# Kernel tuning notes

Measured on AMD Instinct MI355X. Metric: run time of the kernel, lower is better.

The kernel has to match this reference:

```python
import jax, jax.numpy as jnp
import numpy as np

S, D = 8192, 2048      # sequence length, feature dim (input_size)
H, E, K, L = 64, 64, 2, 64  # gate hidden, expert count, top-k, expert layer_size
EPS = 1e-12            # torch F.normalize eps


def setup_inputs() -> dict:
    key = jax.random.key(0)
    ks = jax.random.split(key, 5)
    x = jax.random.normal(ks[0], (S, D), dtype=jnp.float32)
    # torch nn.Linear weights have shape [out_features, in_features]
    Wg_in = jax.random.normal(ks[1], (H, D), dtype=jnp.float32) * 0.02   # gate.input
    Wg_lin = jax.random.normal(ks[2], (E, H), dtype=jnp.float32) * 0.02  # gate.linear
    Wg_out = jax.random.normal(ks[3], (1, S), dtype=jnp.float32) * 0.02  # gate.output
    We = jax.random.normal(ks[4], (E, L, D), dtype=jnp.float32) * 0.02   # expert weight bank
    return {"x": x, "Wg_in": Wg_in, "Wg_lin": Wg_lin, "Wg_out": Wg_out, "We": We}


def reference(x, Wg_in, Wg_lin, Wg_out, We):
    # --- SparseGate (eval mode: dropout = identity) ---
    h = x @ Wg_in.T                         # [S, H]
    logits = h @ Wg_lin.T                   # [S, E]
    scores = (logits.T @ Wg_out.T)[:, 0]    # Linear(S,1) applied to [E,S] -> [E]
    topv, idx = jax.lax.top_k(scores, K)    # global top-k experts for whole input
    g = jax.nn.softmax(topv)                # softmax over the k selected logits

    # --- dispatch to k selected experts (FFNN: Linear -> normalize(-1) -> GELU) ---
    Wsel = We[idx]                          # [K, L, D]
    z = jnp.einsum('sd,kld->ksl', x, Wsel)  # [K, S, L]
    z = z / jnp.maximum(jnp.linalg.norm(z, axis=-1, keepdims=True), EPS)
    z = jax.nn.gelu(z, approximate=False)   # torch GELU default is exact erf

    # --- weighted combine: sum_k g_k * expert_k(x) ---
    return jnp.einsum('k,ksl->sl', g, z)    # [S, L]
```

## Files before the change

### kernel.cpp

```cpp
#include <hip/hip_runtime.h>
#include <hip/hip_bf16.h>
#include <math.h>

#define D_DIM 2048
#define L_DIM 64
#define E_NUM 64
#define H_DIM 64

typedef float f32x4_t __attribute__((ext_vector_type(4)));
typedef __bf16 bf16x8_t __attribute__((ext_vector_type(8)));

#define WS_UPART 0u
#define WS_U     (128u * 2048u * 4u)
#define WS_V     (WS_U + 2048u * 4u)
#define WS_META  (WS_V + 256u)
#define WS_WB    (WS_META + 64u)

__global__ void k_upart(const float* __restrict__ x, const float* __restrict__ wout,
                        float* __restrict__ upart) {
  const int d4 = (blockIdx.x * 256 + threadIdx.x) * 4;
  const int s0 = blockIdx.y * 64;
  const float* xp = x + (size_t)s0 * D_DIM + d4;
  float4 acc = make_float4(0.f, 0.f, 0.f, 0.f);
#pragma unroll 8
  for (int i = 0; i < 64; ++i) {
    const float w = wout[s0 + i];
    const float4 xv = *reinterpret_cast<const float4*>(xp + (size_t)i * D_DIM);
    acc.x += xv.x * w; acc.y += xv.y * w; acc.z += xv.z * w; acc.w += xv.w * w;
  }
  *reinterpret_cast<float4*>(upart + (size_t)blockIdx.y * D_DIM + d4) = acc;
}

__global__ void k_ufinish(const float* __restrict__ upart, float* __restrict__ u) {
  const int d = blockIdx.x * 256 + threadIdx.x;
  float s = 0.f;
#pragma unroll 8
  for (int c = 0; c < 128; ++c) s += upart[(size_t)c * D_DIM + d];
  u[d] = s;
}

__global__ void k_v(const float* __restrict__ wg_in, const float* __restrict__ u,
                    float* __restrict__ v) {
  const int h = blockIdx.x;
  const int t = threadIdx.x;
  const float4* wr = reinterpret_cast<const float4*>(wg_in + (size_t)h * D_DIM);
  const float4* ur = reinterpret_cast<const float4*>(u);
  float s = 0.f;
#pragma unroll
  for (int i = t; i < 512; i += 256) {
    const float4 a = wr[i];
    const float4 b = ur[i];
    s += a.x * b.x + a.y * b.y + a.z * b.z + a.w * b.w;
  }
  __shared__ float red[4];
#pragma unroll
  for (int off = 32; off; off >>= 1) s += __shfl_down(s, off, 64);
  if ((t & 63) == 0) red[t >> 6] = s;
  __syncthreads();
  if (t == 0) v[h] = red[0] + red[1] + red[2] + red[3];
}

__global__ void k_gate(const float* __restrict__ wg_lin, const float* __restrict__ v,
                       int* __restrict__ sel, float* __restrict__ g) {
  __shared__ float vv[H_DIM];
  __shared__ float sc[E_NUM];
  const int t = threadIdx.x;
  vv[t] = v[t];
  __syncthreads();
  float s = 0.f;
#pragma unroll 8
  for (int hh = 0; hh < H_DIM; ++hh) s += wg_lin[t * H_DIM + hh] * vv[hh];
  sc[t] = s;
  __syncthreads();
  if (t == 0) {
    int b1 = 0; float m1 = sc[0];
    for (int e = 1; e < E_NUM; ++e) { if (sc[e] > m1) { m1 = sc[e]; b1 = e; } }
    int b2 = -1; float m2 = -3.4e38f;
    for (int e = 0; e < E_NUM; ++e) {
      if (e != b1 && sc[e] > m2) { m2 = sc[e]; b2 = e; }
    }
    const float e2 = expf(m2 - m1);
    const float g0 = 1.0f / (1.0f + e2);
    sel[0] = b1; sel[1] = b2;
    g[0] = g0; g[1] = 1.0f - g0;
  }
}

__global__ void k_wb(const float* __restrict__ we, const int* __restrict__ sel,
                     __hip_bfloat16* __restrict__ wb) {
  const int n = blockIdx.x;
  const int e = sel[n >> 6];
  const int l = n & 63;
  const float* src = we + ((size_t)e * L_DIM + l) * D_DIM;
  const int t = threadIdx.x;
  const float4 a = reinterpret_cast<const float4*>(src)[2 * t];
  const float4 b = reinterpret_cast<const float4*>(src)[2 * t + 1];
  union { __hip_bfloat16 h[8]; uint4 u; } pk;
  pk.h[0] = __float2bfloat16(a.x); pk.h[1] = __float2bfloat16(a.y);
  pk.h[2] = __float2bfloat16(a.z); pk.h[3] = __float2bfloat16(a.w);
  pk.h[4] = __float2bfloat16(b.x); pk.h[5] = __float2bfloat16(b.y);
  pk.h[6] = __float2bfloat16(b.z); pk.h[7] = __float2bfloat16(b.w);
  reinterpret_cast<uint4*>(wb + (size_t)n * D_DIM)[t] = pk.u;
}

__device__ __forceinline__ void async_ld16(const void* gp, void* lp) {
  __builtin_amdgcn_global_load_lds(
      (const __attribute__((address_space(1))) unsigned int*)gp,
      (__attribute__((address_space(3))) unsigned int*)lp, 16, 0, 0);
}

__device__ __forceinline__ float gelu_f(float v) {
  return 0.5f * v * (1.0f + erff(v * 0.70710678118654752440f));
}

__global__ __launch_bounds__(256) void k_moe_gemm(
    const float* __restrict__ x, const __hip_bfloat16* __restrict__ wb,
    const float* __restrict__ gw, float* __restrict__ out) {
  __shared__ __align__(16) unsigned char lds[32 * 144 + 128 * 64 * 2];
  unsigned char* ldsA0 = lds;
  unsigned char* ldsB0 = lds + 32 * 144;

  const int tid = threadIdx.x;
  const int wv = tid >> 6;
  const int lane = tid & 63;
  const int m0 = blockIdx.x * 32;
  const float g0 = gw[0], g1 = gw[1];

  const int ar = tid >> 3, ac = tid & 7;
  const float* gA = x + (size_t)(m0 + ar) * D_DIM + ac * 8;
  unsigned char* ldsAw = ldsA0 + ar * 144 + ac * 16;

  const int fr = lane & 15, fq = lane >> 4;

  f32x4_t acc00 = {0.f, 0.f, 0.f, 0.f};
  f32x4_t acc01 = acc00, acc10 = acc00, acc11 = acc00;

  for (int kk = 0; kk < D_DIM / 64; ++kk) {
    const int k0 = kk * 64;
    if (kk) __syncthreads();
    const float4 a0 = *reinterpret_cast<const float4*>(gA + k0);
    const float4 a1 = *reinterpret_cast<const float4*>(gA + k0 + 4);
    union { __hip_bfloat16 h[8]; uint4 u; } pk;
    pk.h[0] = __float2bfloat16(a0.x); pk.h[1] = __float2bfloat16(a0.y);
    pk.h[2] = __float2bfloat16(a0.z); pk.h[3] = __float2bfloat16(a0.w);
    pk.h[4] = __float2bfloat16(a1.x); pk.h[5] = __float2bfloat16(a1.y);
    pk.h[6] = __float2bfloat16(a1.z); pk.h[7] = __float2bfloat16(a1.w);
    *reinterpret_cast<uint4*>(ldsAw) = pk.u;
#pragma unroll
    for (int i = 0; i < 4; ++i) {
      const int c = i * 256 + tid;
      const int r = c >> 3, p = c & 7;
      const int kc = p ^ (r & 7);
      async_ld16(wb + (size_t)r * D_DIM + k0 + kc * 8, ldsB0 + c * 16);
    }
    __syncthreads();
    union fragu { uint4 u; bf16x8_t v; };
    fragu af[2][2], bfr[2][2];
#pragma unroll
    for (int mt = 0; mt < 2; ++mt)
#pragma unroll
      for (int ks = 0; ks < 2; ++ks)
        af[mt][ks].u = *reinterpret_cast<const uint4*>(
            ldsA0 + (mt * 16 + fr) * 144 + ks * 64 + fq * 16);
#pragma unroll
    for (int nt = 0; nt < 2; ++nt)
#pragma unroll
      for (int ks = 0; ks < 2; ++ks) {
        const int r = wv * 32 + nt * 16 + fr;
        const int kg = ks * 4 + fq;
        bfr[nt][ks].u = *reinterpret_cast<const uint4*>(
            ldsB0 + r * 128 + ((kg ^ (r & 7)) * 16));
      }
    acc00 = __builtin_amdgcn_mfma_f32_16x16x32_bf16(af[0][0].v, bfr[0][0].v, acc00, 0, 0, 0);
    acc00 = __builtin_amdgcn_mfma_f32_16x16x32_bf16(af[0][1].v, bfr[0][1].v, acc00, 0, 0, 0);
    acc01 = __builtin_amdgcn_mfma_f32_16x16x32_bf16(af[0][0].v, bfr[1][0].v, acc01, 0, 0, 0);
    acc01 = __builtin_amdgcn_mfma_f32_16x16x32_bf16(af[0][1].v, bfr[1][1].v, acc01, 0, 0, 0);
    acc10 = __builtin_amdgcn_mfma_f32_16x16x32_bf16(af[1][0].v, bfr[0][0].v, acc10, 0, 0, 0);
    acc10 = __builtin_amdgcn_mfma_f32_16x16x32_bf16(af[1][1].v, bfr[0][1].v, acc10, 0, 0, 0);
    acc11 = __builtin_amdgcn_mfma_f32_16x16x32_bf16(af[1][0].v, bfr[1][0].v, acc11, 0, 0, 0);
    acc11 = __builtin_amdgcn_mfma_f32_16x16x32_bf16(af[1][1].v, bfr[1][1].v, acc11, 0, 0, 0);
  }
  __syncthreads();
  float* z = reinterpret_cast<float*>(lds);
  {
    const int colbase = wv * 32 + fr;
#pragma unroll
    for (int reg = 0; reg < 4; ++reg) {
      const int r0 = fq * 4 + reg;
      z[r0 * 132 + colbase]             = acc00[reg];
      z[r0 * 132 + colbase + 16]        = acc01[reg];
      z[(16 + r0) * 132 + colbase]      = acc10[reg];
      z[(16 + r0) * 132 + colbase + 16] = acc11[reg];
    }
  }
  __syncthreads();
  float* ps = reinterpret_cast<float*>(lds + 16896);
  {
    const int r = tid >> 3, seg = tid & 7;
    float s = 0.f;
#pragma unroll
    for (int i2 = 0; i2 < 16; ++i2) {
      const float t2 = z[r * 132 + seg * 16 + i2];
      s += t2 * t2;
    }
    ps[r * 8 + seg] = s;
  }
  __syncthreads();
  {
    const int r = tid >> 3, j = tid & 7;
    const float s0 = ps[r * 8 + 0] + ps[r * 8 + 1] + ps[r * 8 + 2] + ps[r * 8 + 3];
    const float s1 = ps[r * 8 + 4] + ps[r * 8 + 5] + ps[r * 8 + 6] + ps[r * 8 + 7];
    const float i0 = 1.0f / fmaxf(sqrtf(s0), 1e-12f);
    const float i1 = 1.0f / fmaxf(sqrtf(s1), 1e-12f);
    float o[8];
#pragma unroll
    for (int i2 = 0; i2 < 8; ++i2) {
      const int c = j * 8 + i2;
      const float za = z[r * 132 + c] * i0;
      const float zb = z[r * 132 + 64 + c] * i1;
      o[i2] = g0 * gelu_f(za) + g1 * gelu_f(zb);
    }
    float4* op = reinterpret_cast<float4*>(out + (size_t)(m0 + r) * 64 + j * 8);
    op[0] = make_float4(o[0], o[1], o[2], o[3]);
    op[1] = make_float4(o[4], o[5], o[6], o[7]);
  }
}

extern "C" void kernel_launch(void* const* d_in, const int* in_sizes, int n_in,
                              void* d_out, int out_size, void* d_ws, size_t ws_size,
                              hipStream_t stream) {
  (void)in_sizes; (void)n_in; (void)out_size; (void)ws_size;
  const float* x      = (const float*)d_in[0];
  const float* wg_in  = (const float*)d_in[1];
  const float* wg_lin = (const float*)d_in[2];
  const float* wg_out = (const float*)d_in[3];
  const float* we     = (const float*)d_in[4];
  float* out = (float*)d_out;
  char* ws = (char*)d_ws;

  float* upart = (float*)(ws + WS_UPART);
  float* u     = (float*)(ws + WS_U);
  float* v     = (float*)(ws + WS_V);
  int*   sel   = (int*)(ws + WS_META);
  float* g     = (float*)(ws + WS_META + 8);
  __hip_bfloat16* wb = (__hip_bfloat16*)(ws + WS_WB);

  k_upart  <<<dim3(2, 128), 256, 0, stream>>>(x, wg_out, upart);
  k_ufinish<<<8, 256, 0, stream>>>(upart, u);
  k_v      <<<64, 256, 0, stream>>>(wg_in, u, v);
  k_gate   <<<1, 64, 0, stream>>>(wg_lin, v, sel, g);
  k_wb     <<<128, 256, 0, stream>>>(we, sel, wb);
  k_moe_gemm<<<256, 256, 0, stream>>>(x, wb, g, out);
}
```

Before: 169.0 us.

## Split GEMM K dimension across four wave groups per block with LDS reduction

The MoE GEMM block grows from 256 to 1024 threads. Each group of 256 threads handles a quarter of the 2048-long reduction using its own LDS staging region, and the partial results are summed in LDS before normalization and GELU. The goal is more in-flight memory traffic and MFMA work per CU with only 256 blocks, which shortens the serial K loop per block. In exchange it adds an LDS reduction step, a larger shared-memory footprint that can lower occupancy, and an epilogue where only a quarter of the threads do work.

```diff
diff --git a/kernel.cpp b/kernel.cpp
--- a/kernel.cpp
+++ b/kernel.cpp
@@ -113,21 +113,26 @@
   return 0.5f * v * (1.0f + erff(v * 0.70710678118654752440f));
 }
 
-__global__ __launch_bounds__(256) void k_moe_gemm(
+#define STG_BYTES 20992
+
+__global__ __launch_bounds__(1024) void k_moe_gemm(
     const float* __restrict__ x, const __hip_bfloat16* __restrict__ wb,
     const float* __restrict__ gw, float* __restrict__ out) {
-  __shared__ __align__(16) unsigned char lds[32 * 144 + 128 * 64 * 2];
-  unsigned char* ldsA0 = lds;
-  unsigned char* ldsB0 = lds + 32 * 144;
+  __shared__ __align__(16) unsigned char lds[4 * STG_BYTES];
 
   const int tid = threadIdx.x;
-  const int wv = tid >> 6;
+  const int kg = tid >> 8;
+  const int lt = tid & 255;
+  const int wc = (tid >> 6) & 3;
   const int lane = tid & 63;
   const int m0 = blockIdx.x * 32;
   const float g0 = gw[0], g1 = gw[1];
 
-  const int ar = tid >> 3, ac = tid & 7;
-  const float* gA = x + (size_t)(m0 + ar) * D_DIM + ac * 8;
+  unsigned char* ldsA0 = lds + kg * STG_BYTES;
+  unsigned char* ldsB0 = ldsA0 + 32 * 144;
+
+  const int ar = lt >> 3, ac = lt & 7;
+  const float* gA = x + (size_t)(m0 + ar) * D_DIM + kg * 512 + ac * 8;
   unsigned char* ldsAw = ldsA0 + ar * 144 + ac * 16;
 
   const int fr = lane & 15, fq = lane >> 4;
@@ -135,11 +140,11 @@
   f32x4_t acc00 = {0.f, 0.f, 0.f, 0.f};
   f32x4_t acc01 = acc00, acc10 = acc00, acc11 = acc00;
 
-  for (int kk = 0; kk < D_DIM / 64; ++kk) {
-    const int k0 = kk * 64;
+  for (int kk = 0; kk < 8; ++kk) {
+    const int k0 = kg * 512 + kk * 64;
     if (kk) __syncthreads();
-    const float4 a0 = *reinterpret_cast<const float4*>(gA + k0);
-    const float4 a1 = *reinterpret_cast<const float4*>(gA + k0 + 4);
+    const float4 a0 = *reinterpret_cast<const float4*>(gA + kk * 64);
+    const float4 a1 = *reinterpret_cast<const float4*>(gA + kk * 64 + 4);
     union { __hip_bfloat16 h[8]; uint4 u; } pk;
     pk.h[0] = __float2bfloat16(a0.x); pk.h[1] = __float2bfloat16(a0.y);
     pk.h[2] = __float2bfloat16(a0.z); pk.h[3] = __float2bfloat16(a0.w);
@@ -148,7 +153,7 @@
     *reinterpret_cast<uint4*>(ldsAw) = pk.u;
 #pragma unroll
     for (int i = 0; i < 4; ++i) {
-      const int c = i * 256 + tid;
+      const int c = i * 256 + lt;
       const int r = c >> 3, p = c & 7;
       const int kc = p ^ (r & 7);
       async_ld16(wb + (size_t)r * D_DIM + k0 + kc * 8, ldsB0 + c * 16);
@@ -166,10 +171,10 @@
     for (int nt = 0; nt < 2; ++nt)
 #pragma unroll
       for (int ks = 0; ks < 2; ++ks) {
-        const int r = wv * 32 + nt * 16 + fr;
-        const int kg = ks * 4 + fq;
+        const int r = wc * 32 + nt * 16 + fr;
+        const int kq = ks * 4 + fq;
         bfr[nt][ks].u = *reinterpret_cast<const uint4*>(
-            ldsB0 + r * 128 + ((kg ^ (r & 7)) * 16));
+            ldsB0 + r * 128 + ((kq ^ (r & 7)) * 16));
       }
     acc00 = __builtin_amdgcn_mfma_f32_16x16x32_bf16(af[0][0].v, bfr[0][0].v, acc00, 0, 0, 0);
     acc00 = __builtin_amdgcn_mfma_f32_16x16x32_bf16(af[0][1].v, bfr[0][1].v, acc00, 0, 0, 0);
@@ -181,9 +186,9 @@
     acc11 = __builtin_amdgcn_mfma_f32_16x16x32_bf16(af[1][1].v, bfr[1][1].v, acc11, 0, 0, 0);
   }
   __syncthreads();
-  float* z = reinterpret_cast<float*>(lds);
   {
-    const int colbase = wv * 32 + fr;
+    float* z = reinterpret_cast<float*>(lds) + kg * (32 * 132);
+    const int colbase = wc * 32 + fr;
 #pragma unroll
     for (int reg = 0; reg < 4; ++reg) {
       const int r0 = fq * 4 + reg;
@@ -194,8 +199,21 @@
     }
   }
   __syncthreads();
-  float* ps = reinterpret_cast<float*>(lds + 16896);
   {
+    float* zb = reinterpret_cast<float*>(lds);
+    const int r = tid >> 5;
+    const int cb = (tid & 31) * 4;
+    const int o = r * 132 + cb;
+    f32x4_t s = *reinterpret_cast<f32x4_t*>(zb + o)
+              + *reinterpret_cast<f32x4_t*>(zb + 1 * 4224 + o)
+              + *reinterpret_cast<f32x4_t*>(zb + 2 * 4224 + o)
+              + *reinterpret_cast<f32x4_t*>(zb + 3 * 4224 + o);
+    *reinterpret_cast<f32x4_t*>(zb + o) = s;
+  }
+  __syncthreads();
+  float* z = reinterpret_cast<float*>(lds);
+  float* ps = reinterpret_cast<float*>(lds + 4 * 16896);
+  if (tid < 256) {
     const int r = tid >> 3, seg = tid & 7;
     float s = 0.f;
 #pragma unroll
@@ -206,7 +224,7 @@
     ps[r * 8 + seg] = s;
   }
   __syncthreads();
-  {
+  if (tid < 256) {
     const int r = tid >> 3, j = tid & 7;
     const float s0 = ps[r * 8 + 0] + ps[r * 8 + 1] + ps[r * 8 + 2] + ps[r * 8 + 3];
     const float s1 = ps[r * 8 + 4] + ps[r * 8 + 5] + ps[r * 8 + 6] + ps[r * 8 + 7];
@@ -250,5 +268,5 @@
   k_v      <<<64, 256, 0, stream>>>(wg_in, u, v);
   k_gate   <<<1, 64, 0, stream>>>(wg_lin, v, sel, g);
   k_wb     <<<128, 256, 0, stream>>>(we, sel, wb);
-  k_moe_gemm<<<256, 256, 0, stream>>>(x, wb, g, out);
-}
+  k_moe_gemm<<<256, 1024, 0, stream>>>(x, wb, g, out);
+}
```

Result: faster. 159.3 us (-5.8%).
